# Optimization experiments

Measured on AMD Instinct MI355X. Metric: run time of the kernel, lower is better.

The kernel has to match this reference:

```python
import jax, jax.numpy as jnp
import numpy as np

IN_CH, D, K = 256, 128, 512

def setup_inputs() -> dict:
    key = jax.random.key(0)
    k1, k2, k3, k4 = jax.random.split(key, 4)
    x = jax.random.normal(k1, (16, IN_CH, 64, 64), dtype=jnp.float32)
    W = jax.random.normal(k2, (D, IN_CH), dtype=jnp.float32) * (1.0 / np.sqrt(IN_CH))
    b = jax.random.normal(k3, (D,), dtype=jnp.float32) * 0.01
    prototypes = jax.random.normal(k4, (K, D), dtype=jnp.float32) * 0.02
    gamma = jnp.asarray(1.0, dtype=jnp.float32)
    return {"x": x, "W": W, "b": b, "prototypes": prototypes, "gamma": gamma}

def reference(x, W, b, prototypes, gamma):
    n, c, h, w = x.shape
    # 1x1 conv projection: [n,c,h,w] -> [n,h,w,d]
    q = jnp.einsum('nchw,dc->nhwd', x, W) + b
    q_flat = q.reshape(n * h * w, -1)                      # [T, d]
    q_norm2 = jnp.sum(q_flat * q_flat, axis=1, keepdims=True)   # [T, 1]
    p_norm2 = jnp.sum(prototypes * prototypes, axis=1)[None, :] # [1, K]
    dist2 = q_norm2 + p_norm2 - 2.0 * (q_flat @ prototypes.T)   # [T, K]
    weights = jax.nn.softmax(-jnp.abs(gamma) * dist2, axis=1)
    return weights.reshape(n, h, w, -1).transpose(0, 3, 1, 2)   # [n, K, h, w]
```

## Files before the change

### kernel.cpp

```cpp
#include <hip/hip_runtime.h>

#define HW 4096
#define NCH 256
#define DIM 128
#define NPROTO 512

typedef __attribute__((ext_vector_type(4))) float f32x4;
typedef __attribute__((ext_vector_type(8))) short s16x8;

__device__ __forceinline__ unsigned short f2bf(float f) {
  union { float f; unsigned u; } v; v.f = f;
  unsigned r = v.u + 0x7fffu + ((v.u >> 16) & 1u);
  return (unsigned short)(r >> 16);
}

__device__ __forceinline__ void gload_lds16(const void* g, void* l) {
  __builtin_amdgcn_global_load_lds(
      (const __attribute__((address_space(1))) void*)g,
      (__attribute__((address_space(3))) void*)l, 16, 0, 0);
}

__global__ __launch_bounds__(256) void prep_kernel(const float* __restrict__ P,
                                                   const float* __restrict__ Wm,
                                                   unsigned short* __restrict__ Pr,
                                                   unsigned short* __restrict__ Wbf,
                                                   float* __restrict__ pn2) {
  const int tid = threadIdx.x;
  const int b = blockIdx.x;
  if (b < 8) {
    const int n  = b * 64 + (tid >> 2);
    const int qt = tid & 3;
    const float* row = P + n * DIM + qt * 32;
    unsigned short* dst = Pr + ((size_t)qt * NPROTO + n) * 32;
    float ssq = 0.f;
#pragma unroll
    for (int u = 0; u < 8; ++u) {
      f32x4 v = *(const f32x4*)(row + 4 * u);
      ssq += v.x * v.x + v.y * v.y + v.z * v.z + v.w * v.w;
      dst[4 * u + 0] = f2bf(v.x);
      dst[4 * u + 1] = f2bf(v.y);
      dst[4 * u + 2] = f2bf(v.z);
      dst[4 * u + 3] = f2bf(v.w);
    }
    ssq += __shfl_xor(ssq, 1);
    ssq += __shfl_xor(ssq, 2);
    if (qt == 0) pn2[n] = ssq;
  } else {
    const int idx = ((b - 8) * 256 + tid) * 16;
#pragma unroll
    for (int u = 0; u < 4; ++u) {
      f32x4 v = *(const f32x4*)(Wm + idx + 4 * u);
      unsigned short* d = Wbf + idx + 4 * u;
      d[0] = f2bf(v.x); d[1] = f2bf(v.y); d[2] = f2bf(v.z); d[3] = f2bf(v.w);
    }
  }
}

__global__ __launch_bounds__(512, 4) void fused_kernel(
    const float* __restrict__ x, const unsigned short* __restrict__ Wbf,
    const float* __restrict__ bias, const unsigned short* __restrict__ Pr,
    const float* __restrict__ pn2, const float* __restrict__ gptr,
    float* __restrict__ out) {
  __shared__ __align__(16) char smem[61440];
  unsigned short* q_s = (unsigned short*)smem;
  char*           x_b = smem + 17408;
  unsigned short* w_s = (unsigned short*)(smem + 17408 + 9216);
  unsigned short* P_s = (unsigned short*)(smem + 17408);
  float* red  = (float*)(smem + 58880);
  float* rmx  = (float*)(smem + 60928);
  float* rinv = (float*)(smem + 61184);

  const int tid  = threadIdx.x;
  const int p0   = blockIdx.x * 64;
  const int nimg = p0 >> 12;
  const int hw0  = p0 & 4095;
  const int wave = tid >> 6, lane = tid & 63;
  const int l15 = lane & 15, l4 = lane >> 4;
  const int wr = wave >> 2, wc = wave & 3;

  f32x4 acc1[2][2];
#pragma unroll
  for (int i = 0; i < 2; ++i)
#pragma unroll
    for (int j = 0; j < 2; ++j)
#pragma unroll
      for (int r = 0; r < 4; ++r) acc1[i][j][r] = 0.f;

  const float* xb = x + (size_t)nimg * NCH * HW + hw0;
  const int f  = tid & 15;
  const int cp = tid >> 4;
  const int wrow = 8 * wave + (lane >> 3);
  const int wu   = lane & 7;

  for (int c0 = 0; c0 < NCH; c0 += 64) {
#pragma unroll
    for (int t = 0; t < 2; ++t) {
      const int row = 64 * t + wrow;
      const unsigned short* src =
          Wbf + (size_t)row * NCH + c0 + ((wu ^ (row & 7)) << 3);
      gload_lds16(src, (char*)w_s + t * 8192 + wave * 1024);
    }
    f32x4 v0 = *(const f32x4*)(xb + (size_t)(c0 + 2 * cp + 0) * HW + 4 * f);
    f32x4 v1 = *(const f32x4*)(xb + (size_t)(c0 + 2 * cp + 1) * HW + 4 * f);
#pragma unroll
    for (int s = 0; s < 4; ++s) {
      const int row = 4 * f + s;
      unsigned pk = (unsigned)f2bf(v0[s]) | ((unsigned)f2bf(v1[s]) << 16);
      *(unsigned*)(x_b + row * 144 + ((4 * cp) ^ (((row >> 2) & 7) << 4))) = pk;
    }
    __syncthreads();
#pragma unroll
    for (int kc = 0; kc < 64; kc += 32) {
      const int ub = (kc >> 3) + l4;
      s16x8 a[2];
#pragma unroll
      for (int i = 0; i < 2; ++i) {
        const int row = 32 * wr + 16 * i + l15;
        a[i] = *(const s16x8*)(x_b + row * 144 + 16 * (ub ^ ((row >> 2) & 7)));
      }
#pragma unroll
      for (int j = 0; j < 2; ++j) {
        s16x8 b = *(const s16x8*)&w_s[(32 * wc + 16 * j + l15) * 64 +
                                      ((ub ^ (l15 & 7)) << 3)];
#pragma unroll
        for (int i = 0; i < 2; ++i)
          acc1[i][j] = __builtin_amdgcn_mfma_f32_16x16x32_bf16(a[i], b, acc1[i][j], 0, 0, 0);
      }
    }
    __syncthreads();
  }

#pragma unroll
  for (int j = 0; j < 2; ++j) {
    const int d = 32 * wc + 16 * j + l15;
    const float bv = bias[d];
#pragma unroll
    for (int i = 0; i < 2; ++i) {
      const int px = 32 * wr + 16 * i + 4 * l4;
#pragma unroll
      for (int r = 0; r < 4; ++r)
        q_s[(px + r) * 136 + d] = f2bf(acc1[i][j][r] + bv);
    }
  }

  s16x8 pf[4];
  {
    const unsigned short* ps = Pr + (size_t)tid * 32;
#pragma unroll
    for (int u = 0; u < 4; ++u) pf[u] = *(const s16x8*)(ps + 8 * u);
  }

  f32x4 acc[4][4];
#pragma unroll
  for (int i = 0; i < 4; ++i)
#pragma unroll
    for (int j = 0; j < 4; ++j)
#pragma unroll
      for (int r = 0; r < 4; ++r) acc[i][j][r] = 0.f;

  for (int ch = 0; ch < 4; ++ch) {
    __syncthreads();
    {
      unsigned short* dst = &P_s[tid * 40];
#pragma unroll
      for (int u = 0; u < 4; ++u) *(s16x8*)(dst + 8 * u) = pf[u];
    }
    __syncthreads();
    if (ch < 3) {
      const unsigned short* ps = Pr + (size_t)((ch + 1) * NPROTO + tid) * 32;
#pragma unroll
      for (int u = 0; u < 4; ++u) pf[u] = *(const s16x8*)(ps + 8 * u);
    }
    const int dk = 32 * ch;
    s16x8 afr[4];
#pragma unroll
    for (int i = 0; i < 4; ++i)
      afr[i] = *(const s16x8*)&q_s[(16 * i + l15) * 136 + dk + 8 * l4];
#pragma unroll
    for (int j = 0; j < 4; ++j) {
      s16x8 bfr = *(const s16x8*)&P_s[(64 * wave + 16 * j + l15) * 40 + 8 * l4];
#pragma unroll
      for (int i = 0; i < 4; ++i)
        acc[i][j] = __builtin_amdgcn_mfma_f32_16x16x32_bf16(afr[i], bfr, acc[i][j], 0, 0, 0);
    }
  }

  const float g2  = fabsf(gptr[0]) * 1.44269504088896340736f;
  const float tg2 = 2.f * g2;
  float cj[4];
#pragma unroll
  for (int j = 0; j < 4; ++j) cj[j] = g2 * pn2[64 * wave + 16 * j + l15];

#pragma unroll
  for (int i = 0; i < 4; ++i)
#pragma unroll
    for (int r = 0; r < 4; ++r) {
      float m = -1e30f;
#pragma unroll
      for (int j = 0; j < 4; ++j) {
        float lv = fmaf(acc[i][j][r], tg2, -cj[j]);
        acc[i][j][r] = lv;
        m = fmaxf(m, lv);
      }
#pragma unroll
      for (int s = 1; s < 16; s <<= 1) m = fmaxf(m, __shfl_xor(m, s));
      if (l15 == 0) red[wave * 64 + 16 * i + 4 * l4 + r] = m;
    }
  __syncthreads();
  if (tid < 64) {
    float M = red[tid];
#pragma unroll
    for (int w = 1; w < 8; ++w) M = fmaxf(M, red[w * 64 + tid]);
    rmx[tid] = M;
  }
  __syncthreads();

#pragma unroll
  for (int i = 0; i < 4; ++i) {
    const f32x4 Mi = *(const f32x4*)&rmx[16 * i + 4 * l4];
#pragma unroll
    for (int r = 0; r < 4; ++r) {
      float s = 0.f;
#pragma unroll
      for (int j = 0; j < 4; ++j) {
        float e = exp2f(acc[i][j][r] - Mi[r]);
        acc[i][j][r] = e;
        s += e;
      }
#pragma unroll
      for (int t = 1; t < 16; t <<= 1) s += __shfl_xor(s, t);
      if (l15 == 0) red[wave * 64 + 16 * i + 4 * l4 + r] = s;
    }
  }
  __syncthreads();
  if (tid < 64) {
    float S = 0.f;
#pragma unroll
    for (int w = 0; w < 8; ++w) S += red[w * 64 + tid];
    rinv[tid] = 1.f / S;
  }
  __syncthreads();

  float* ob = out + (size_t)nimg * NPROTO * HW + hw0;
#pragma unroll
  for (int i = 0; i < 4; ++i) {
    const f32x4 iv = *(const f32x4*)&rinv[16 * i + 4 * l4];
    const int px = 16 * i + 4 * l4;
#pragma unroll
    for (int j = 0; j < 4; ++j) {
      const int k = 64 * wave + 16 * j + l15;
      f32x4 o = acc[i][j] * iv;
      *(f32x4*)(ob + (size_t)k * HW + px) = o;
    }
  }
}

extern "C" void kernel_launch(void* const* d_in, const int* in_sizes, int n_in,
                              void* d_out, int out_size, void* d_ws, size_t ws_size,
                              hipStream_t stream) {
  const float* x     = (const float*)d_in[0];
  const float* Wm    = (const float*)d_in[1];
  const float* bias  = (const float*)d_in[2];
  const float* prot  = (const float*)d_in[3];
  const float* gamma = (const float*)d_in[4];
  float* out = (float*)d_out;

  unsigned short* Pr_w  = (unsigned short*)d_ws;
  float*          pn2_w = (float*)((char*)d_ws + 131072);
  unsigned short* W_ws  = (unsigned short*)((char*)d_ws + 131072 + 2048);

  prep_kernel<<<16, 256, 0, stream>>>(prot, Wm, Pr_w, W_ws, pn2_w);
  fused_kernel<<<1024, 512, 0, stream>>>(x, W_ws, bias, Pr_w, pn2_w, gamma, out);
}
```

Measured before the change: 215.5 us.

## Double-buffer projection GEMM stages and stream prototypes per-wave via direct LDS loads

The projection GEMM's channel loop now double-buffers both the W tile (async global-to-LDS) and the x tile, prefetching the next chunk while the current one is computed. Explicit waitcnt plus raw barriers replace the paired __syncthreads. Prototype chunks are loaded per wave straight into private LDS regions with global_load_lds, which removes the register staging and two block barriers per chunk. q_s gets an XOR swizzle instead of padding. This uses more LDS, which may lower occupancy, and the hand-written vmcnt counts must match the outstanding loads exactly.

```diff
diff --git a/kernel.cpp b/kernel.cpp
--- a/kernel.cpp
+++ b/kernel.cpp
@@ -61,14 +61,14 @@
     const float* __restrict__ bias, const unsigned short* __restrict__ Pr,
     const float* __restrict__ pn2, const float* __restrict__ gptr,
     float* __restrict__ out) {
-  __shared__ __align__(16) char smem[61440];
+  __shared__ __align__(16) char smem[70144];
   unsigned short* q_s = (unsigned short*)smem;
-  char*           x_b = smem + 17408;
-  unsigned short* w_s = (unsigned short*)(smem + 17408 + 9216);
-  unsigned short* P_s = (unsigned short*)(smem + 17408);
-  float* red  = (float*)(smem + 58880);
-  float* rmx  = (float*)(smem + 60928);
-  float* rinv = (float*)(smem + 61184);
+  char* x_b = smem + 16384;
+  char* wsb = smem + 16384 + 18432;
+  char* P_w = smem + 16384;
+  float* red  = (float*)(smem + 67584);
+  float* rmx  = (float*)(smem + 69632);
+  float* rinv = (float*)(smem + 69888);
 
   const int tid  = threadIdx.x;
   const int p0   = blockIdx.x * 64;
@@ -92,23 +92,42 @@
   const int wrow = 8 * wave + (lane >> 3);
   const int wu   = lane & 7;
 
-  for (int c0 = 0; c0 < NCH; c0 += 64) {
-#pragma unroll
-    for (int t = 0; t < 2; ++t) {
-      const int row = 64 * t + wrow;
-      const unsigned short* src =
-          Wbf + (size_t)row * NCH + c0 + ((wu ^ (row & 7)) << 3);
-      gload_lds16(src, (char*)w_s + t * 8192 + wave * 1024);
-    }
-    f32x4 v0 = *(const f32x4*)(xb + (size_t)(c0 + 2 * cp + 0) * HW + 4 * f);
-    f32x4 v1 = *(const f32x4*)(xb + (size_t)(c0 + 2 * cp + 1) * HW + 4 * f);
+#pragma unroll
+  for (int t = 0; t < 2; ++t) {
+    const int row = 64 * t + wrow;
+    gload_lds16(Wbf + (size_t)row * NCH + ((wu ^ (row & 7)) << 3),
+                wsb + t * 8192 + wave * 1024);
+  }
+  f32x4 cv0 = *(const f32x4*)(xb + (size_t)(2 * cp + 0) * HW + 4 * f);
+  f32x4 cv1 = *(const f32x4*)(xb + (size_t)(2 * cp + 1) * HW + 4 * f);
+
+#pragma unroll
+  for (int it = 0; it < 4; ++it) {
+    const int buf = it & 1;
+    const int c0n = 64 * (it + 1);
+    if (it < 3) {
+#pragma unroll
+      for (int t = 0; t < 2; ++t) {
+        const int row = 64 * t + wrow;
+        gload_lds16(Wbf + (size_t)row * NCH + c0n + ((wu ^ (row & 7)) << 3),
+                    wsb + (buf ^ 1) * 16384 + t * 8192 + wave * 1024);
+      }
+    }
+    f32x4 nv0 = cv0, nv1 = cv1;
+    if (it < 3) {
+      nv0 = *(const f32x4*)(xb + (size_t)(c0n + 2 * cp + 0) * HW + 4 * f);
+      nv1 = *(const f32x4*)(xb + (size_t)(c0n + 2 * cp + 1) * HW + 4 * f);
+    }
 #pragma unroll
     for (int s = 0; s < 4; ++s) {
       const int row = 4 * f + s;
-      unsigned pk = (unsigned)f2bf(v0[s]) | ((unsigned)f2bf(v1[s]) << 16);
-      *(unsigned*)(x_b + row * 144 + ((4 * cp) ^ (((row >> 2) & 7) << 4))) = pk;
-    }
-    __syncthreads();
+      unsigned pk = (unsigned)f2bf(cv0[s]) | ((unsigned)f2bf(cv1[s]) << 16);
+      *(unsigned*)(x_b + buf * 9216 + row * 144 +
+                   ((4 * cp) ^ (((row >> 2) & 7) << 4))) = pk;
+    }
+    if (it < 3) asm volatile("s_waitcnt vmcnt(4) lgkmcnt(0)" ::: "memory");
+    else        asm volatile("s_waitcnt vmcnt(0) lgkmcnt(0)" ::: "memory");
+    __builtin_amdgcn_s_barrier();
 #pragma unroll
     for (int kc = 0; kc < 64; kc += 32) {
       const int ub = (kc >> 3) + l4;
@@ -116,39 +135,46 @@
 #pragma unroll
       for (int i = 0; i < 2; ++i) {
         const int row = 32 * wr + 16 * i + l15;
-        a[i] = *(const s16x8*)(x_b + row * 144 + 16 * (ub ^ ((row >> 2) & 7)));
+        a[i] = *(const s16x8*)(x_b + buf * 9216 + row * 144 +
+                               16 * (ub ^ ((row >> 2) & 7)));
       }
 #pragma unroll
       for (int j = 0; j < 2; ++j) {
-        s16x8 b = *(const s16x8*)&w_s[(32 * wc + 16 * j + l15) * 64 +
-                                      ((ub ^ (l15 & 7)) << 3)];
+        s16x8 b = *(const s16x8*)(wsb + buf * 16384 +
+                                  (32 * wc + 16 * j + l15) * 128 +
+                                  ((ub ^ (l15 & 7)) << 4));
 #pragma unroll
         for (int i = 0; i < 2; ++i)
           acc1[i][j] = __builtin_amdgcn_mfma_f32_16x16x32_bf16(a[i], b, acc1[i][j], 0, 0, 0);
       }
     }
-    __syncthreads();
-  }
+    asm volatile("s_waitcnt lgkmcnt(0)" ::: "memory");
+    __builtin_amdgcn_s_barrier();
+    cv0 = nv0; cv1 = nv1;
+  }
+
+#pragma unroll
+  for (int t = 0; t < 4; ++t)
+    gload_lds16(Pr + (size_t)(64 * wave + 16 * t) * 32 + 8 * lane,
+                P_w + wave * 4096 + t * 1024);
 
 #pragma unroll
   for (int j = 0; j < 2; ++j) {
     const int d = 32 * wc + 16 * j + l15;
     const float bv = bias[d];
+    const int u  = d >> 3;
+    const int d7 = d & 7;
 #pragma unroll
     for (int i = 0; i < 2; ++i) {
-      const int px = 32 * wr + 16 * i + 4 * l4;
-#pragma unroll
-      for (int r = 0; r < 4; ++r)
-        q_s[(px + r) * 136 + d] = f2bf(acc1[i][j][r] + bv);
-    }
-  }
-
-  s16x8 pf[4];
-  {
-    const unsigned short* ps = Pr + (size_t)tid * 32;
-#pragma unroll
-    for (int u = 0; u < 4; ++u) pf[u] = *(const s16x8*)(ps + 8 * u);
-  }
+      const int pxb = 32 * wr + 16 * i + 4 * l4;
+#pragma unroll
+      for (int r = 0; r < 4; ++r) {
+        const int px = pxb + r;
+        q_s[px * 128 + ((u ^ (px & 7)) << 3) + d7] = f2bf(acc1[i][j][r] + bv);
+      }
+    }
+  }
+  __syncthreads();
 
   f32x4 acc[4][4];
 #pragma unroll
@@ -158,30 +184,30 @@
 #pragma unroll
       for (int r = 0; r < 4; ++r) acc[i][j][r] = 0.f;
 
+  const unsigned short* Pw = (const unsigned short*)(P_w + wave * 4096);
+
+#pragma unroll
   for (int ch = 0; ch < 4; ++ch) {
-    __syncthreads();
-    {
-      unsigned short* dst = &P_s[tid * 40];
-#pragma unroll
-      for (int u = 0; u < 4; ++u) *(s16x8*)(dst + 8 * u) = pf[u];
-    }
-    __syncthreads();
-    if (ch < 3) {
-      const unsigned short* ps = Pr + (size_t)((ch + 1) * NPROTO + tid) * 32;
-#pragma unroll
-      for (int u = 0; u < 4; ++u) pf[u] = *(const s16x8*)(ps + 8 * u);
-    }
-    const int dk = 32 * ch;
+    if (ch) asm volatile("s_waitcnt vmcnt(0)" ::: "memory");
     s16x8 afr[4];
 #pragma unroll
-    for (int i = 0; i < 4; ++i)
-      afr[i] = *(const s16x8*)&q_s[(16 * i + l15) * 136 + dk + 8 * l4];
+    for (int i = 0; i < 4; ++i) {
+      const int px = 16 * i + l15;
+      afr[i] = *(const s16x8*)&q_s[px * 128 + (((4 * ch + l4) ^ (l15 & 7)) << 3)];
+    }
 #pragma unroll
     for (int j = 0; j < 4; ++j) {
-      s16x8 bfr = *(const s16x8*)&P_s[(64 * wave + 16 * j + l15) * 40 + 8 * l4];
+      s16x8 bfr = *(const s16x8*)&Pw[(16 * j + l15) * 32 + 8 * l4];
 #pragma unroll
       for (int i = 0; i < 4; ++i)
         acc[i][j] = __builtin_amdgcn_mfma_f32_16x16x32_bf16(afr[i], bfr, acc[i][j], 0, 0, 0);
+    }
+    if (ch < 3) {
+      __builtin_amdgcn_sched_barrier(0);
+#pragma unroll
+      for (int t = 0; t < 4; ++t)
+        gload_lds16(Pr + (size_t)((ch + 1) * NPROTO + 64 * wave + 16 * t) * 32 + 8 * lane,
+                    P_w + wave * 4096 + t * 1024);
     }
   }
 
```

Result: no change. 213.8 us (-0.8%).
